# Performance work log

Hardware: AMD Instinct MI355X
Metric: run time of the kernel (lower is better)

Reference implementation:

```python
import jax, jax.numpy as jnp
import numpy as np

B, TV, TH, F, H, D = 16, 128, 64, 512, 512, 256


def setup_inputs() -> dict:
    key = jax.random.key(0)
    ks = jax.random.split(key, 6)
    return {
        "v": jax.random.normal(ks[0], (B, TV, F), dtype=jnp.float32),
        "h": jax.random.normal(ks[1], (B, TH, H), dtype=jnp.float32),
        "W": jax.random.normal(ks[2], (F, D), dtype=jnp.float32) * 0.05,
        "U": jax.random.normal(ks[3], (H, D), dtype=jnp.float32) * 0.05,
        "b": jax.random.normal(ks[4], (D,), dtype=jnp.float32) * 0.05,
        "w": jax.random.normal(ks[5], (D, 1), dtype=jnp.float32) * 0.05,
    }


def reference(v, h, W, U, b, w):
    # v: [B, Tv, F] video features; h: [B, Th, H] decoder hidden states
    Wv = jnp.einsum("btf,fd->btd", v, W)      # [B, Tv, D]
    Uh = jnp.einsum("bsh,hd->bsd", h, U)      # [B, Th, D]
    # Broadcast add -> [B, Th, Tv, D], tanh nonlinearity (additive attention)
    f = jnp.tanh(Uh[:, :, None, :] + Wv[:, None, :, :] + b)
    q = jnp.einsum("bstd,d->bst", f, w[:, 0])  # scores [B, Th, Tv]
    beta = jax.nn.softmax(q, axis=-1)           # softmax over Tv (axis -2 of q[..., None])
    u = jnp.einsum("bst,btf->bsf", beta, v)    # context [B, Th, F]
    return u
```

## Files before the change

### kernel.cpp

```cpp
#include <hip/hip_runtime.h>
#include <hip/hip_bf16.h>

#define BB 16
#define TV 128
#define TH 64
#define FF 512
#define HH 512
#define DD 256

#define LOG2E2 2.8853900817779268f

typedef __attribute__((ext_vector_type(8))) short bf16x8;
typedef __attribute__((ext_vector_type(4))) float f32x4;

__device__ __forceinline__ float fast_exp2(float x) {
#if __has_builtin(__builtin_amdgcn_exp2f)
  return __builtin_amdgcn_exp2f(x);
#else
  return __expf(x * 0.6931471805599453f);
#endif
}
__device__ __forceinline__ float fast_rcp(float x) {
#if __has_builtin(__builtin_amdgcn_rcpf)
  return __builtin_amdgcn_rcpf(x);
#else
  return 1.0f / x;
#endif
}
__device__ __forceinline__ unsigned short f2bf(float x) {
  union { float f; unsigned u; } a; a.f = x;
  unsigned r = a.u + 0x7fffu + ((a.u >> 16) & 1u);
  return (unsigned short)(r >> 16);
}

#define NT_V 262144
#define NT_H 131072
#define NT_W 32768
__global__ __launch_bounds__(256) void convert_kernel(
    const float* __restrict__ v, const float* __restrict__ h,
    const float* __restrict__ W, const float* __restrict__ U,
    unsigned short* __restrict__ vb, unsigned short* __restrict__ hb,
    unsigned short* __restrict__ WT, unsigned short* __restrict__ UT) {
  int task = blockIdx.x * 256 + threadIdx.x;
  if (task < NT_V) {
    float4 x = ((const float4*)v)[task];
    ushort4 o = make_ushort4(f2bf(x.x), f2bf(x.y), f2bf(x.z), f2bf(x.w));
    *(ushort4*)&vb[(size_t)task * 4] = o;
  } else if (task < NT_V + NT_H) {
    int t2 = task - NT_V;
    float4 x = ((const float4*)h)[t2];
    ushort4 o = make_ushort4(f2bf(x.x), f2bf(x.y), f2bf(x.z), f2bf(x.w));
    *(ushort4*)&hb[(size_t)t2 * 4] = o;
  } else {
    int t2 = task - NT_V - NT_H;
    const float* S;
    unsigned short* Dt;
    if (t2 < NT_W) { S = W; Dt = WT; } else { S = U; Dt = UT; t2 -= NT_W; }
    int n = t2 & 255, k4 = t2 >> 8;
    float a0 = S[(k4 * 4 + 0) * 256 + n];
    float a1 = S[(k4 * 4 + 1) * 256 + n];
    float a2 = S[(k4 * 4 + 2) * 256 + n];
    float a3 = S[(k4 * 4 + 3) * 256 + n];
    ushort4 o = make_ushort4(f2bf(a0), f2bf(a1), f2bf(a2), f2bf(a3));
    *(ushort4*)&Dt[(size_t)n * 512 + k4 * 4] = o;
  }
}

__global__ __launch_bounds__(128) void mfma_gemm_kernel(
    const unsigned short* __restrict__ Av, const unsigned short* __restrict__ Ah,
    const unsigned short* __restrict__ WT, const unsigned short* __restrict__ UT,
    const float* __restrict__ bias, float* __restrict__ Wv2T,
    float* __restrict__ Uh2) {
  const int bid = blockIdx.x;
  const unsigned short* A;
  const unsigned short* BT;
  int mt, nt;
  bool is_wv;
  if (bid < 256) {
    A = Av; BT = WT; is_wv = true;
    mt = bid >> 3; nt = bid & 7;
  } else {
    const int b2 = bid - 256;
    A = Ah; BT = UT; is_wv = false;
    mt = b2 >> 3; nt = b2 & 7;
  }
  const int wv   = threadIdx.x >> 6;
  const int lane = threadIdx.x & 63;
  const int m0   = mt * 64 + wv * 32;
  const int n0   = nt * 32;
  const int r16  = lane & 15;
  const int quad = lane >> 4;

  const unsigned short* a0p = A + (size_t)(m0 + r16) * 512 + quad * 8;
  const unsigned short* a1p = a0p + 16 * 512;
  const unsigned short* b0p = BT + (size_t)(n0 + r16) * 512 + quad * 8;
  const unsigned short* b1p = b0p + 16 * 512;

  f32x4 acc00 = {0.f, 0.f, 0.f, 0.f};
  f32x4 acc01 = {0.f, 0.f, 0.f, 0.f};
  f32x4 acc10 = {0.f, 0.f, 0.f, 0.f};
  f32x4 acc11 = {0.f, 0.f, 0.f, 0.f};

#pragma unroll
  for (int kc = 0; kc < 16; kc++) {
    bf16x8 a0 = *(const bf16x8*)(a0p + kc * 32);
    bf16x8 a1 = *(const bf16x8*)(a1p + kc * 32);
    bf16x8 b0 = *(const bf16x8*)(b0p + kc * 32);
    bf16x8 b1 = *(const bf16x8*)(b1p + kc * 32);
    acc00 = __builtin_amdgcn_mfma_f32_16x16x32_bf16(a0, b0, acc00, 0, 0, 0);
    acc01 = __builtin_amdgcn_mfma_f32_16x16x32_bf16(a0, b1, acc01, 0, 0, 0);
    acc10 = __builtin_amdgcn_mfma_f32_16x16x32_bf16(a1, b0, acc10, 0, 0, 0);
    acc11 = __builtin_amdgcn_mfma_f32_16x16x32_bf16(a1, b1, acc11, 0, 0, 0);
  }

  if (is_wv) {
    const int bb   = m0 >> 7;
    const int tb   = (m0 & 127) + quad * 4;
    float* Wb = Wv2T + (size_t)bb * 32768;
#pragma unroll
    for (int r = 0; r < 4; r++) {
      Wb[(size_t)(n0 + r16) * 128 + tb + r]        = acc00[r] * LOG2E2;
      Wb[(size_t)(n0 + 16 + r16) * 128 + tb + r]   = acc01[r] * LOG2E2;
      Wb[(size_t)(n0 + r16) * 128 + tb + 16 + r]   = acc10[r] * LOG2E2;
      Wb[(size_t)(n0 + 16 + r16) * 128 + tb + 16 + r] = acc11[r] * LOG2E2;
    }
  } else {
    const float bj0 = bias[n0 + r16];
    const float bj1 = bias[n0 + 16 + r16];
#pragma unroll
    for (int r = 0; r < 4; r++) {
      const int row0 = m0 + quad * 4 + r;
      Uh2[(size_t)row0 * 256 + n0 + r16]             = (acc00[r] + bj0) * LOG2E2;
      Uh2[(size_t)row0 * 256 + n0 + 16 + r16]        = (acc01[r] + bj1) * LOG2E2;
      Uh2[(size_t)(row0 + 16) * 256 + n0 + r16]      = (acc10[r] + bj0) * LOG2E2;
      Uh2[(size_t)(row0 + 16) * 256 + n0 + 16 + r16] = (acc11[r] + bj1) * LOG2E2;
    }
  }
}

__global__ __launch_bounds__(1024) void attn_fused_kernel(
    const float* __restrict__ Wv2T, const float* __restrict__ Uh2,
    const float* __restrict__ wg, const float* __restrict__ v,
    float* __restrict__ u) {
  __shared__ float UhS[4 * 256];
  __shared__ float wS[256];
  __shared__ float pS[4 * 1024];
  __shared__ float bS[4 * 128];
  __shared__ float mW[8];
  __shared__ float sW[8];

  const int tid = threadIdx.x;
  const int b   = blockIdx.x >> 4;
  const int sg  = blockIdx.x & 15;
  const int s0  = sg * 4;

  if (tid < 256) {
    const int row = tid >> 6, q4 = (tid & 63) << 2;
    *(float4*)&UhS[row * 256 + q4] =
        *(const float4*)&Uh2[(size_t)(b * 64 + s0 + row) * 256 + q4];
  } else if (tid < 320) {
    const int q4 = (tid - 256) << 2;
    *(float4*)&wS[q4] = *(const float4*)&wg[q4];
  }
  __syncthreads();

  {
    const int t4 = tid & 31;
    const int dg = (tid >> 5) & 7;
    const int s  = tid >> 8;
    const float* wvb = Wv2T + (size_t)b * 32768 + (size_t)dg * 32 * 128 + t4 * 4;
    const float* uhp = &UhS[s * 256 + dg * 32];
    const float* wp  = &wS[dg * 32];
    float4 acc = {0.f, 0.f, 0.f, 0.f};
#pragma unroll 8
    for (int j = 0; j < 32; j++) {
      float4 a  = *(const float4*)(wvb + j * 128);
      float uh = uhp[j];
      float ww = wp[j];
      acc.x = fmaf(ww, fast_rcp(fast_exp2(a.x + uh) + 1.0f), acc.x);
      acc.y = fmaf(ww, fast_rcp(fast_exp2(a.y + uh) + 1.0f), acc.y);
      acc.z = fmaf(ww, fast_rcp(fast_exp2(a.z + uh) + 1.0f), acc.z);
      acc.w = fmaf(ww, fast_rcp(fast_exp2(a.w + uh) + 1.0f), acc.w);
    }
    *(float4*)&pS[s * 1024 + dg * 128 + t4 * 4] = acc;
  }
  __syncthreads();

  float qv = 0.0f, ev = 0.0f;
  const int wvid = tid >> 6, lane = tid & 63;
  if (tid < 512) {
    const int s_l = tid >> 7, t = tid & 127;
    float ssum = 0.0f;
#pragma unroll
    for (int dg = 0; dg < 8; dg++) ssum += pS[s_l * 1024 + dg * 128 + t];
    qv = ssum * (-LOG2E2);
    float m = qv;
#pragma unroll
    for (int off = 32; off > 0; off >>= 1) m = fmaxf(m, __shfl_xor(m, off, 64));
    if (lane == 0) mW[wvid] = m;
  }
  __syncthreads();
  if (tid < 512) {
    float m = fmaxf(mW[wvid], mW[wvid ^ 1]);
    ev = fast_exp2(qv - m);
    float ssum = ev;
#pragma unroll
    for (int off = 32; off > 0; off >>= 1) ssum += __shfl_xor(ssum, off, 64);
    if (lane == 0) sW[wvid] = ssum;
  }
  __syncthreads();
  if (tid < 512) {
    const int s_l = tid >> 7, t = tid & 127;
    bS[s_l * 128 + t] = ev * fast_rcp(sW[wvid] + sW[wvid ^ 1]);
  }
  __syncthreads();

  const float* vb2 = v + (size_t)b * TV * FF;
  const int f  = tid & 511;
  const int sh = tid >> 9;
  float a0 = 0.f, a1 = 0.f;
#pragma unroll 4
  for (int tg = 0; tg < 128; tg += 4) {
    float4 b0 = *(const float4*)&bS[(sh * 2 + 0) * 128 + tg];
    float4 b1 = *(const float4*)&bS[(sh * 2 + 1) * 128 + tg];
    float v0 = vb2[(tg + 0) * 512 + f];
    float v1 = vb2[(tg + 1) * 512 + f];
    float v2 = vb2[(tg + 2) * 512 + f];
    float v3 = vb2[(tg + 3) * 512 + f];
    a0 = fmaf(b0.x, v0, a0); a0 = fmaf(b0.y, v1, a0);
    a0 = fmaf(b0.z, v2, a0); a0 = fmaf(b0.w, v3, a0);
    a1 = fmaf(b1.x, v0, a1); a1 = fmaf(b1.y, v1, a1);
    a1 = fmaf(b1.z, v2, a1); a1 = fmaf(b1.w, v3, a1);
  }
  float* urow = u + (size_t)(b * 64 + s0 + sh * 2) * 512;
  urow[0 * 512 + f] = a0;
  urow[1 * 512 + f] = a1;
}

extern "C" void kernel_launch(void* const* d_in, const int* in_sizes, int n_in,
                              void* d_out, int out_size, void* d_ws, size_t ws_size,
                              hipStream_t stream) {
  const float* v  = (const float*)d_in[0];
  const float* h  = (const float*)d_in[1];
  const float* W  = (const float*)d_in[2];
  const float* U  = (const float*)d_in[3];
  const float* bb = (const float*)d_in[4];
  const float* w  = (const float*)d_in[5];
  float* u = (float*)d_out;

  float* Wv2T = (float*)d_ws;
  float* Uh2  = Wv2T + (size_t)2048 * 256;
  unsigned short* vb16 = (unsigned short*)(Uh2 + (size_t)1024 * 256);
  unsigned short* hb16 = vb16 + (size_t)2048 * 512;
  unsigned short* WT   = hb16 + (size_t)1024 * 512;
  unsigned short* UT   = WT + (size_t)256 * 512;

  convert_kernel<<<1792, 256, 0, stream>>>(v, h, W, U, vb16, hb16, WT, UT);
  mfma_gemm_kernel<<<384, 128, 0, stream>>>(vb16, hb16, WT, UT, bb, Wv2T, Uh2);
  attn_fused_kernel<<<256, 1024, 0, stream>>>(Wv2T, Uh2, w, v, u);
}
```

Baseline: 93.09 us.

## Factor exp out of tanh scores and pair reciprocals in attention kernel

The GEMM epilogue now stores exp2 of the scaled Wv and Uh terms, so each score term becomes 1/(1+Ea*Eu) without a per-element exp. The attention kernel combines two d-terms over a common denominator, which halves the reciprocals. It also restructures the thread mapping so each thread handles all four decoder rows with register-held Eu/w, reduces across half-waves via shuffle, and remaps block-to-batch order. Large pre-activations can overflow exp2 or the product D0*D1, which risks inf/NaN or precision loss.

After: 90.78 us. -2.5%, faster.

```diff
diff --git a/kernel.cpp b/kernel.cpp
--- a/kernel.cpp
+++ b/kernel.cpp
@@ -69,8 +69,8 @@
 __global__ __launch_bounds__(128) void mfma_gemm_kernel(
     const unsigned short* __restrict__ Av, const unsigned short* __restrict__ Ah,
     const unsigned short* __restrict__ WT, const unsigned short* __restrict__ UT,
-    const float* __restrict__ bias, float* __restrict__ Wv2T,
-    float* __restrict__ Uh2) {
+    const float* __restrict__ bias, float* __restrict__ EaT,
+    float* __restrict__ EuhT) {
   const int bid = blockIdx.x;
   const unsigned short* A;
   const unsigned short* BT;
@@ -116,13 +116,13 @@
   if (is_wv) {
     const int bb   = m0 >> 7;
     const int tb   = (m0 & 127) + quad * 4;
-    float* Wb = Wv2T + (size_t)bb * 32768;
+    float* Wb = EaT + (size_t)bb * 32768;
 #pragma unroll
     for (int r = 0; r < 4; r++) {
-      Wb[(size_t)(n0 + r16) * 128 + tb + r]        = acc00[r] * LOG2E2;
-      Wb[(size_t)(n0 + 16 + r16) * 128 + tb + r]   = acc01[r] * LOG2E2;
-      Wb[(size_t)(n0 + r16) * 128 + tb + 16 + r]   = acc10[r] * LOG2E2;
-      Wb[(size_t)(n0 + 16 + r16) * 128 + tb + 16 + r] = acc11[r] * LOG2E2;
+      Wb[(size_t)(n0 + r16) * 128 + tb + r]           = fast_exp2(acc00[r] * LOG2E2);
+      Wb[(size_t)(n0 + 16 + r16) * 128 + tb + r]      = fast_exp2(acc01[r] * LOG2E2);
+      Wb[(size_t)(n0 + r16) * 128 + tb + 16 + r]      = fast_exp2(acc10[r] * LOG2E2);
+      Wb[(size_t)(n0 + 16 + r16) * 128 + tb + 16 + r] = fast_exp2(acc11[r] * LOG2E2);
     }
   } else {
     const float bj0 = bias[n0 + r16];
@@ -130,34 +130,36 @@
 #pragma unroll
     for (int r = 0; r < 4; r++) {
       const int row0 = m0 + quad * 4 + r;
-      Uh2[(size_t)row0 * 256 + n0 + r16]             = (acc00[r] + bj0) * LOG2E2;
-      Uh2[(size_t)row0 * 256 + n0 + 16 + r16]        = (acc01[r] + bj1) * LOG2E2;
-      Uh2[(size_t)(row0 + 16) * 256 + n0 + r16]      = (acc10[r] + bj0) * LOG2E2;
-      Uh2[(size_t)(row0 + 16) * 256 + n0 + 16 + r16] = (acc11[r] + bj1) * LOG2E2;
+      EuhT[(size_t)row0 * 256 + n0 + r16]             = fast_exp2((acc00[r] + bj0) * LOG2E2);
+      EuhT[(size_t)row0 * 256 + n0 + 16 + r16]        = fast_exp2((acc01[r] + bj1) * LOG2E2);
+      EuhT[(size_t)(row0 + 16) * 256 + n0 + r16]      = fast_exp2((acc10[r] + bj0) * LOG2E2);
+      EuhT[(size_t)(row0 + 16) * 256 + n0 + 16 + r16] = fast_exp2((acc11[r] + bj1) * LOG2E2);
     }
   }
 }
 
 __global__ __launch_bounds__(1024) void attn_fused_kernel(
-    const float* __restrict__ Wv2T, const float* __restrict__ Uh2,
+    const float* __restrict__ EaT, const float* __restrict__ EuhT,
     const float* __restrict__ wg, const float* __restrict__ v,
     float* __restrict__ u) {
-  __shared__ float UhS[4 * 256];
+  __shared__ float EuhS[4 * 256];
   __shared__ float wS[256];
-  __shared__ float pS[4 * 1024];
+  __shared__ float pS[4 * 16 * 128];
   __shared__ float bS[4 * 128];
   __shared__ float mW[8];
   __shared__ float sW[8];
 
   const int tid = threadIdx.x;
-  const int b   = blockIdx.x >> 4;
-  const int sg  = blockIdx.x & 15;
-  const int s0  = sg * 4;
+  const int bid  = blockIdx.x;
+  const int slot = bid >> 3;
+  const int b    = (bid & 7) * 2 + (slot >> 4);
+  const int sg   = slot & 15;
+  const int s0   = sg * 4;
 
   if (tid < 256) {
     const int row = tid >> 6, q4 = (tid & 63) << 2;
-    *(float4*)&UhS[row * 256 + q4] =
-        *(const float4*)&Uh2[(size_t)(b * 64 + s0 + row) * 256 + q4];
+    *(float4*)&EuhS[row * 256 + q4] =
+        *(const float4*)&EuhT[(size_t)(b * 64 + s0 + row) * 256 + q4];
   } else if (tid < 320) {
     const int q4 = (tid - 256) << 2;
     *(float4*)&wS[q4] = *(const float4*)&wg[q4];
@@ -165,24 +167,61 @@
   __syncthreads();
 
   {
-    const int t4 = tid & 31;
-    const int dg = (tid >> 5) & 7;
-    const int s  = tid >> 8;
-    const float* wvb = Wv2T + (size_t)b * 32768 + (size_t)dg * 32 * 128 + t4 * 4;
-    const float* uhp = &UhS[s * 256 + dg * 32];
-    const float* wp  = &wS[dg * 32];
-    float4 acc = {0.f, 0.f, 0.f, 0.f};
-#pragma unroll 8
-    for (int j = 0; j < 32; j++) {
-      float4 a  = *(const float4*)(wvb + j * 128);
-      float uh = uhp[j];
-      float ww = wp[j];
-      acc.x = fmaf(ww, fast_rcp(fast_exp2(a.x + uh) + 1.0f), acc.x);
-      acc.y = fmaf(ww, fast_rcp(fast_exp2(a.y + uh) + 1.0f), acc.y);
-      acc.z = fmaf(ww, fast_rcp(fast_exp2(a.z + uh) + 1.0f), acc.z);
-      acc.w = fmaf(ww, fast_rcp(fast_exp2(a.w + uh) + 1.0f), acc.w);
-    }
-    *(float4*)&pS[s * 1024 + dg * 128 + t4 * 4] = acc;
+    const int t4  = tid & 31;
+    const int dgf = tid >> 5;
+    const float* eab = EaT + (size_t)b * 32768 + (size_t)dgf * 8 * 128 + t4 * 4;
+
+    float eu[4][8];
+    float wr[8];
+#pragma unroll
+    for (int s = 0; s < 4; s++) {
+      *(float4*)&eu[s][0] = *(const float4*)&EuhS[s * 256 + dgf * 8];
+      *(float4*)&eu[s][4] = *(const float4*)&EuhS[s * 256 + dgf * 8 + 4];
+    }
+    *(float4*)&wr[0] = *(const float4*)&wS[dgf * 8];
+    *(float4*)&wr[4] = *(const float4*)&wS[dgf * 8 + 4];
+
+    f32x4 acc[4];
+#pragma unroll
+    for (int s = 0; s < 4; s++) acc[s] = (f32x4){0.f, 0.f, 0.f, 0.f};
+
+#pragma unroll
+    for (int jp = 0; jp < 4; jp++) {
+      float4 e0 = *(const float4*)(eab + (2 * jp + 0) * 128);
+      float4 e1 = *(const float4*)(eab + (2 * jp + 1) * 128);
+      const float w0 = wr[2 * jp], w1 = wr[2 * jp + 1];
+#pragma unroll
+      for (int s = 0; s < 4; s++) {
+        const float u0 = eu[s][2 * jp], u1 = eu[s][2 * jp + 1];
+        float D0, D1, num;
+        D0 = fmaf(e0.x, u0, 1.0f); D1 = fmaf(e1.x, u1, 1.0f);
+        num = fmaf(w1, D0, w0 * D1);
+        acc[s][0] = fmaf(num, fast_rcp(D0 * D1), acc[s][0]);
+        D0 = fmaf(e0.y, u0, 1.0f); D1 = fmaf(e1.y, u1, 1.0f);
+        num = fmaf(w1, D0, w0 * D1);
+        acc[s][1] = fmaf(num, fast_rcp(D0 * D1), acc[s][1]);
+        D0 = fmaf(e0.z, u0, 1.0f); D1 = fmaf(e1.z, u1, 1.0f);
+        num = fmaf(w1, D0, w0 * D1);
+        acc[s][2] = fmaf(num, fast_rcp(D0 * D1), acc[s][2]);
+        D0 = fmaf(e0.w, u0, 1.0f); D1 = fmaf(e1.w, u1, 1.0f);
+        num = fmaf(w1, D0, w0 * D1);
+        acc[s][3] = fmaf(num, fast_rcp(D0 * D1), acc[s][3]);
+      }
+    }
+
+#pragma unroll
+    for (int s = 0; s < 4; s++) {
+#pragma unroll
+      for (int c = 0; c < 4; c++) acc[s][c] += __shfl_xor(acc[s][c], 32, 64);
+    }
+    const int wv_ = tid >> 6;
+    if ((tid & 63) < 32) {
+#pragma unroll
+      for (int s = 0; s < 4; s++) {
+        float4 o = make_float4(acc[s][0], acc[s][1], acc[s][2], acc[s][3]);
+        *(float4*)&pS[(s * 16 + wv_) * 128 + t4 * 4] = o;
+      }
+    }
   }
   __syncthreads();
 
@@ -192,7 +231,7 @@
     const int s_l = tid >> 7, t = tid & 127;
     float ssum = 0.0f;
 #pragma unroll
-    for (int dg = 0; dg < 8; dg++) ssum += pS[s_l * 1024 + dg * 128 + t];
+    for (int k = 0; k < 16; k++) ssum += pS[(s_l * 16 + k) * 128 + t];
     qv = ssum * (-LOG2E2);
     float m = qv;
 #pragma unroll
@@ -248,14 +287,14 @@
   const float* w  = (const float*)d_in[5];
   float* u = (float*)d_out;
 
-  float* Wv2T = (float*)d_ws;
-  float* Uh2  = Wv2T + (size_t)2048 * 256;
-  unsigned short* vb16 = (unsigned short*)(Uh2 + (size_t)1024 * 256);
+  float* EaT  = (float*)d_ws;
+  float* EuhT = EaT + (size_t)2048 * 256;
+  unsigned short* vb16 = (unsigned short*)(EuhT + (size_t)1024 * 256);
   unsigned short* hb16 = vb16 + (size_t)2048 * 512;
   unsigned short* WT   = hb16 + (size_t)1024 * 512;
   unsigned short* UT   = WT + (size_t)256 * 512;
 
   convert_kernel<<<1792, 256, 0, stream>>>(v, h, W, U, vb16, hb16, WT, UT);
-  mfma_gemm_kernel<<<384, 128, 0, stream>>>(vb16, hb16, WT, UT, bb, Wv2T, Uh2);
-  attn_fused_kernel<<<256, 1024, 0, stream>>>(Wv2T, Uh2, w, v, u);
-}
+  mfma_gemm_kernel<<<384, 128, 0, stream>>>(vb16, hb16, WT, UT, bb, EaT, EuhT);
+  attn_fused_kernel<<<256, 1024, 0, stream>>>(EaT, EuhT, w, v, u);
+}
```
